# Kernel optimization log

Hardware: AMD Instinct MI355X
Metric: run time of the kernel (lower is better)

Reference implementation:

```python
import jax, jax.numpy as jnp
import numpy as np
import math

B, S, D, H = 4, 2048, 1024, 16
HD = D // H  # 64
MOD_DIMS = [("text", 768, 2048), ("image", 1024, 1024), ("audio", 512, 1500), ("video", 2048, 512)]
M = len(MOD_DIMS)
WIN, DEPTH = 3, 8


def _cantor_routes():
    coords = []
    for i in range(M):
        x = i / max(1, M - 1)
        x = max(1e-06, min(x, 1.0 - 1e-06))
        val, f = 0.0, 0.5
        for _ in range(DEPTH):
            x *= 3.0
            d = int(x)
            x -= d
            if d == 2:
                val += f
            f *= 0.5
        coords.append(val)
    c = np.asarray(coords, dtype=np.float32)
    dist = np.abs(c[:, None] - c[None, :])
    # topk smallest distances (stable tie-break like torch ascending sort)
    return np.argsort(dist, axis=1, kind="stable")[:, :WIN]

ROUTES = jnp.asarray(_cantor_routes())


def setup_inputs() -> dict:
    key = jax.random.key(0)
    ks = iter(jax.random.split(key, 32))
    inp = {}
    for name, dim, sl in MOD_DIMS:
        inp[name] = jax.random.normal(next(ks), (B, sl, dim), dtype=jnp.float32)
        inp[f"W_{name}"] = jax.random.normal(next(ks), (D, dim), dtype=jnp.float32) / math.sqrt(dim)
        inp[f"b_{name}"] = jnp.zeros((D,), dtype=jnp.float32)
    inp["mod_emb"] = jax.random.normal(next(ks), (M, D), dtype=jnp.float32) * 0.02
    for nm in ("q", "k", "v", "o"):
        inp[f"W{nm}"] = jax.random.normal(next(ks), (D, D), dtype=jnp.float32) / math.sqrt(D)
        inp[f"b{nm}"] = jnp.zeros((D,), dtype=jnp.float32)
    inp["temperature"] = jnp.asarray(0.07, dtype=jnp.float32)
    return inp


def reference(text, image, audio, video, W_text, b_text, W_image, b_image,
              W_audio, b_audio, W_video, b_video, mod_emb, Wq, bq, Wk, bk,
              Wv, bv, Wo, bo, temperature):
    xs = [text, image, audio, video]
    Ws = [W_text, W_image, W_audio, W_video]
    bs = [b_text, b_image, b_audio, b_video]
    projected = []
    for i in range(M):
        p = xs[i] @ Ws[i].T + bs[i] + mod_emb[i]          # [B, s_i, D]
        p = jnp.pad(p, ((0, 0), (0, S - p.shape[1]), (0, 0)))
        projected.append(p)
    stacked = jnp.stack(projected, axis=1)                # [B, M, S, D]

    def heads(x, W, b):
        return (x @ W.T + b).reshape(B, M, S, H, HD).transpose(0, 3, 1, 2, 4)  # [B,H,M,S,HD]

    Q = heads(stacked, Wq, bq)
    K = heads(stacked, Wk, bk)
    V = heads(stacked, Wv, bv)

    Kn = K[:, :, ROUTES]
    Vn = V[:, :, ROUTES]
    scores = jnp.einsum('bhmsd,bhmwsd->bhmsw', Q, Kn) / (math.sqrt(HD) * jnp.abs(temperature))
    attn = jax.nn.softmax(scores, axis=-1)                # dropout is identity at eval
    out = jnp.einsum('bhmsw,bhmwsd->bhmsd', attn, Vn)     # [B,H,M,S,HD]
    fused = out.mean(axis=2)                              # [B,H,S,HD]
    fused = fused.transpose(0, 2, 1, 3).reshape(B, S, D)
    return fused @ Wo.T + bo
```

## Files before the change

### kernel.cpp

```cpp
#include <hip/hip_runtime.h>

typedef unsigned short u16;
typedef __bf16 bf16x8 __attribute__((ext_vector_type(8)));
typedef u16   u16x8  __attribute__((ext_vector_type(8)));
typedef u16   u16x4  __attribute__((ext_vector_type(4)));
typedef float f32x4  __attribute__((ext_vector_type(4)));

#define RPB 5084
#define SL0 2048
#define SL1 1024
#define SL2 1500
#define SL3 512

__device__ __forceinline__ u16 f2bf(float f) {
  union { float f; unsigned u; } x; x.f = f;
  unsigned u = x.u;
  u += 0x7fffu + ((u >> 16) & 1u);
  return (u16)(u >> 16);
}
__device__ __forceinline__ float bf2f(u16 h) {
  union { unsigned u; float f; } x; x.u = ((unsigned)h) << 16;
  return x.f;
}
__device__ __forceinline__ void gll16(const u16* g, u16* l) {
  __builtin_amdgcn_global_load_lds(
      (const __attribute__((address_space(1))) void*)g,
      (__attribute__((address_space(3))) void*)l, 16, 0, 0);
}

#define NSEG 12
struct CvtSegs {
  const float* src[NSEG];
  u16*         dst[NSEG];
  int          blk_end[NSEG];
  int          blk_base[NSEG];
};
__global__ __launch_bounds__(256) void cvt_multi(CvtSegs segs) {
  int blk = blockIdx.x, seg = 0;
#pragma unroll
  for (int s = 0; s < NSEG; ++s) if (blk >= segs.blk_end[s]) seg = s + 1;
  const float* src = segs.src[seg];
  u16* dst = segs.dst[seg];
  int i = (blk - segs.blk_base[seg]) * 1024 + threadIdx.x * 4;
  f32x4 v = *(const f32x4*)(src + i);
  u16x4 o;
  o[0] = f2bf(v[0]); o[1] = f2bf(v[1]); o[2] = f2bf(v[2]); o[3] = f2bf(v[3]);
  *(u16x4*)(dst + i) = o;
}


template<int STORE_F32>
__global__ __launch_bounds__(256) void gemm_lds(
    const u16* __restrict__ A,
    const u16* __restrict__ B0, const u16* __restrict__ B1, const u16* __restrict__ B2,
    const float* __restrict__ c0, const float* __restrict__ c1, const float* __restrict__ c2,
    void* __restrict__ Cout, int Mr, int K, int ldc)
{
  __shared__ u16 lA0[128 * 32], lA1[128 * 32];
  __shared__ u16 lB0[128 * 32], lB1[128 * 32];
  const int tid  = threadIdx.x;
  const int lane = tid & 63;
  const int wave = tid >> 6;
  const int wr   = (wave >> 1) * 64;
  const int wc   = (wave & 1) * 64;
  const int row0 = blockIdx.y * 128;

  const int wsel = blockIdx.x >> 3;
  const int colL = (blockIdx.x & 7) * 128;
  const u16*   Bw   = (wsel == 0) ? B0 : (wsel == 1) ? B1 : B2;
  const float* bias = (wsel == 0) ? c0 : (wsel == 1) ? c1 : c2;

  const int sr  = wave * 32 + (lane >> 2);
  const int sc  = (lane & 3) * 8;
  int ra0 = row0 + sr;      if (ra0 >= Mr) ra0 = Mr - 1;
  int ra1 = row0 + sr + 16; if (ra1 >= Mr) ra1 = Mr - 1;
  const u16* pA0 = A + (size_t)ra0 * K + sc;
  const u16* pA1 = A + (size_t)ra1 * K + sc;
  const u16* pB0 = Bw + (size_t)(colL + sr) * K + sc;
  const u16* pB1 = pB0 + (size_t)16 * K;
  u16* dA0a = &lA0[(wave * 32) * 32];      u16* dA1a = &lA0[(wave * 32 + 16) * 32];
  u16* dA0b = &lA1[(wave * 32) * 32];      u16* dA1b = &lA1[(wave * 32 + 16) * 32];
  u16* dB0a = &lB0[(wave * 32) * 32];      u16* dB1a = &lB0[(wave * 32 + 16) * 32];
  u16* dB0b = &lB1[(wave * 32) * 32];      u16* dB1b = &lB1[(wave * 32 + 16) * 32];

  f32x4 acc[4][4];
#pragma unroll
  for (int i = 0; i < 4; ++i)
#pragma unroll
    for (int j = 0; j < 4; ++j) acc[i][j] = f32x4{0.f, 0.f, 0.f, 0.f};

  const int fr = lane & 15;
  const int fk = (lane >> 4) * 8;

  for (int k0 = 0; k0 < K; k0 += 64) {
    __syncthreads();
    gll16(pA0 + k0, dA0a);       gll16(pA1 + k0, dA1a);
    gll16(pB0 + k0, dB0a);       gll16(pB1 + k0, dB1a);
    gll16(pA0 + k0 + 32, dA0b);  gll16(pA1 + k0 + 32, dA1b);
    gll16(pB0 + k0 + 32, dB0b);  gll16(pB1 + k0 + 32, dB1b);
    __syncthreads();

    bf16x8 af[4], bfr[4];
#pragma unroll
    for (int i = 0; i < 4; ++i)
      af[i] = *(const bf16x8*)&lA0[(wr + i * 16 + fr) * 32 + fk];
#pragma unroll
    for (int j = 0; j < 4; ++j)
      bfr[j] = *(const bf16x8*)&lB0[(wc + j * 16 + fr) * 32 + fk];
#pragma unroll
    for (int i = 0; i < 4; ++i)
#pragma unroll
      for (int j = 0; j < 4; ++j)
        acc[i][j] = __builtin_amdgcn_mfma_f32_16x16x32_bf16(af[i], bfr[j], acc[i][j], 0, 0, 0);
#pragma unroll
    for (int i = 0; i < 4; ++i)
      af[i] = *(const bf16x8*)&lA1[(wr + i * 16 + fr) * 32 + fk];
#pragma unroll
    for (int j = 0; j < 4; ++j)
      bfr[j] = *(const bf16x8*)&lB1[(wc + j * 16 + fr) * 32 + fk];
#pragma unroll
    for (int i = 0; i < 4; ++i)
#pragma unroll
      for (int j = 0; j < 4; ++j)
        acc[i][j] = __builtin_amdgcn_mfma_f32_16x16x32_bf16(af[i], bfr[j], acc[i][j], 0, 0, 0);
  }

  const int fc = lane & 15;
  const int rq = (lane >> 4) * 4;
#pragma unroll
  for (int i = 0; i < 4; ++i) {
#pragma unroll
    for (int j = 0; j < 4; ++j) {
      const int cl = wc + j * 16 + fc;
      const float badd = bias[colL + cl];
      const int gc = blockIdx.x * 128 + cl;
#pragma unroll
      for (int reg = 0; reg < 4; ++reg) {
        int gr = row0 + wr + i * 16 + rq + reg;
        if (gr < Mr) {
          float v = acc[i][j][reg] + badd;
          if (STORE_F32) ((float*)Cout)[(size_t)gr * ldc + gc] = v;
          else           ((u16*)Cout)[(size_t)gr * ldc + gc] = f2bf(v);
        }
      }
    }
  }
}

struct ProjSegs {
  const u16*   A[4];
  const u16*   Bw[4];
  const float* b0[4];
  const float* b1[4];
  int Mr[4], K[4], sl[4], obase[4];
  int blk_end[4];
};
__global__ __launch_bounds__(256) void gemm_proj_all(ProjSegs ps, u16* __restrict__ Cout) {
  int blk = blockIdx.x, seg = 0;
#pragma unroll
  for (int s = 0; s < 3; ++s) if (blk >= ps.blk_end[s]) seg = s + 1;
  const int base  = seg ? ps.blk_end[seg - 1] : 0;
  const int local = blk - base;
  const int row0  = (local >> 3) * 128;
  const int col0  = (local & 7) * 128;
  const int Mr = ps.Mr[seg], K = ps.K[seg], sl = ps.sl[seg], obase = ps.obase[seg];
  const u16* A  = ps.A[seg];
  const u16* Bw = ps.Bw[seg];
  const float* bias0 = ps.b0[seg];
  const float* bias1 = ps.b1[seg];

  __shared__ u16 lA0[128 * 32], lA1[128 * 32];
  __shared__ u16 lB0[128 * 32], lB1[128 * 32];
  const int tid  = threadIdx.x;
  const int lane = tid & 63;
  const int wave = tid >> 6;
  const int wr   = (wave >> 1) * 64;
  const int wc   = (wave & 1) * 64;

  const int sr  = wave * 32 + (lane >> 2);
  const int sc  = (lane & 3) * 8;
  int ra0 = row0 + sr;      if (ra0 >= Mr) ra0 = Mr - 1;
  int ra1 = row0 + sr + 16; if (ra1 >= Mr) ra1 = Mr - 1;
  const u16* pA0 = A + (size_t)ra0 * K + sc;
  const u16* pA1 = A + (size_t)ra1 * K + sc;
  const u16* pB0 = Bw + (size_t)(col0 + sr) * K + sc;
  const u16* pB1 = pB0 + (size_t)16 * K;
  u16* dA0a = &lA0[(wave * 32) * 32];      u16* dA1a = &lA0[(wave * 32 + 16) * 32];
  u16* dA0b = &lA1[(wave * 32) * 32];      u16* dA1b = &lA1[(wave * 32 + 16) * 32];
  u16* dB0a = &lB0[(wave * 32) * 32];      u16* dB1a = &lB0[(wave * 32 + 16) * 32];
  u16* dB0b = &lB1[(wave * 32) * 32];      u16* dB1b = &lB1[(wave * 32 + 16) * 32];

  f32x4 acc[4][4];
#pragma unroll
  for (int i = 0; i < 4; ++i)
#pragma unroll
    for (int j = 0; j < 4; ++j) acc[i][j] = f32x4{0.f, 0.f, 0.f, 0.f};

  const int fr = lane & 15;
  const int fk = (lane >> 4) * 8;

  for (int k0 = 0; k0 < K; k0 += 64) {
    __syncthreads();
    gll16(pA0 + k0, dA0a);       gll16(pA1 + k0, dA1a);
    gll16(pB0 + k0, dB0a);       gll16(pB1 + k0, dB1a);
    gll16(pA0 + k0 + 32, dA0b);  gll16(pA1 + k0 + 32, dA1b);
    gll16(pB0 + k0 + 32, dB0b);  gll16(pB1 + k0 + 32, dB1b);
    __syncthreads();

    bf16x8 af[4], bfr[4];
#pragma unroll
    for (int i = 0; i < 4; ++i)
      af[i] = *(const bf16x8*)&lA0[(wr + i * 16 + fr) * 32 + fk];
#pragma unroll
    for (int j = 0; j < 4; ++j)
      bfr[j] = *(const bf16x8*)&lB0[(wc + j * 16 + fr) * 32 + fk];
#pragma unroll
    for (int i = 0; i < 4; ++i)
#pragma unroll
      for (int j = 0; j < 4; ++j)
        acc[i][j] = __builtin_amdgcn_mfma_f32_16x16x32_bf16(af[i], bfr[j], acc[i][j], 0, 0, 0);
#pragma unroll
    for (int i = 0; i < 4; ++i)
      af[i] = *(const bf16x8*)&lA1[(wr + i * 16 + fr) * 32 + fk];
#pragma unroll
    for (int j = 0; j < 4; ++j)
      bfr[j] = *(const bf16x8*)&lB1[(wc + j * 16 + fr) * 32 + fk];
#pragma unroll
    for (int i = 0; i < 4; ++i)
#pragma unroll
      for (int j = 0; j < 4; ++j)
        acc[i][j] = __builtin_amdgcn_mfma_f32_16x16x32_bf16(af[i], bfr[j], acc[i][j], 0, 0, 0);
  }

  const int fc = lane & 15;
  const int rq = (lane >> 4) * 4;
#pragma unroll
  for (int i = 0; i < 4; ++i) {
#pragma unroll
    for (int j = 0; j < 4; ++j) {
      const int c = col0 + wc + j * 16 + fc;
      const float badd = bias0[c] + bias1[c];
#pragma unroll
      for (int reg = 0; reg < 4; ++reg) {
        int gr = row0 + wr + i * 16 + rq + reg;
        if (gr < Mr) {
          int bb = gr / sl, ss = gr - bb * sl;
          Cout[(size_t)(bb * RPB + obase + ss) * 1024 + c] = f2bf(acc[i][j][reg] + badd);
        }
      }
    }
  }
}

__global__ __launch_bounds__(256) void attn_fuse(
    const u16* __restrict__ QKV,
    u16* __restrict__ fused,
    const float* __restrict__ bq, const float* __restrict__ bk, const float* __restrict__ bv,
    const float* __restrict__ temp_ptr)
{
  const int ROUTE[4][3] = {{0,1,2},{0,1,2},{2,3,0},{3,2,0}};
  const int SLm[4]  = {SL0, SL1, SL2, SL3};
  const int OFFS[4] = {0, 2048, 3072, 4572};
  const int tid  = threadIdx.x;
  const int lane = tid & 63;
  const int wave = tid >> 6;
  const int bs   = blockIdx.x * 2 + (wave >> 1);
  const int s    = bs & 2047;
  const int b    = bs >> 11;
  const int h    = (wave & 1) * 8 + (lane >> 3);
  const int sub  = lane & 7;
  const int dbase = h * 64 + sub * 8;
  const float scale = 1.0f / (8.0f * fabsf(temp_ptr[0]));

  float qf[4][8], kf[4][8], vf[4][8];
#pragma unroll
  for (int r = 0; r < 4; ++r) {
    if (s < SLm[r]) {
      const u16* base = QKV + ((size_t)(b * RPB + OFFS[r] + s)) * 3072 + dbase;
      u16x8 q8 = *(const u16x8*)(base);
      u16x8 k8 = *(const u16x8*)(base + 1024);
      u16x8 v8 = *(const u16x8*)(base + 2048);
#pragma unroll
      for (int i = 0; i < 8; ++i) {
        qf[r][i] = bf2f(q8[i]); kf[r][i] = bf2f(k8[i]); vf[r][i] = bf2f(v8[i]);
      }
    } else {
#pragma unroll
      for (int i = 0; i < 8; ++i) {
        qf[r][i] = bq[dbase + i]; kf[r][i] = bk[dbase + i]; vf[r][i] = bv[dbase + i];
      }
    }
  }

  float acc[8];
#pragma unroll
  for (int i = 0; i < 8; ++i) acc[i] = 0.f;

#pragma unroll
  for (int m = 0; m < 4; ++m) {
    float sc[3];
#pragma unroll
    for (int w = 0; w < 3; ++w) {
      const int r = ROUTE[m][w];
      float d = 0.f;
#pragma unroll
      for (int i = 0; i < 8; ++i) d += qf[m][i] * kf[r][i];
      d += __shfl_xor(d, 1, 64);
      d += __shfl_xor(d, 2, 64);
      d += __shfl_xor(d, 4, 64);
      sc[w] = d * scale;
    }
    float mx = fmaxf(sc[0], fmaxf(sc[1], sc[2]));
    float e0 = __expf(sc[0] - mx), e1 = __expf(sc[1] - mx), e2 = __expf(sc[2] - mx);
    float inv = 1.0f / (e0 + e1 + e2);
    float ws[3] = {e0 * inv, e1 * inv, e2 * inv};
#pragma unroll
    for (int w = 0; w < 3; ++w) {
      const int r = ROUTE[m][w];
#pragma unroll
      for (int i = 0; i < 8; ++i) acc[i] += ws[w] * vf[r][i];
    }
  }
  u16x8 o;
#pragma unroll
  for (int i = 0; i < 8; ++i) o[i] = f2bf(acc[i] * 0.25f);
  *(u16x8*)(fused + (size_t)bs * 1024 + dbase) = o;
}

extern "C" void kernel_launch(void* const* d_in, const int* in_sizes, int n_in,
                              void* d_out, int out_size, void* d_ws, size_t ws_size,
                              hipStream_t stream) {
  const int B = 4, S = 2048, D = 1024;
  const int SL[4]   = {SL0, SL1, SL2, SL3};
  const int DIM[4]  = {768, 1024, 512, 2048};
  const int OFFS[4] = {0, 2048, 3072, 4572};

  const float* x[4]  = {(const float*)d_in[0], (const float*)d_in[3], (const float*)d_in[6], (const float*)d_in[9]};
  const float* Wm[4] = {(const float*)d_in[1], (const float*)d_in[4], (const float*)d_in[7], (const float*)d_in[10]};
  const float* bm[4] = {(const float*)d_in[2], (const float*)d_in[5], (const float*)d_in[8], (const float*)d_in[11]};
  const float* mod_emb = (const float*)d_in[12];
  const float* Wq = (const float*)d_in[13]; const float* bq = (const float*)d_in[14];
  const float* Wk = (const float*)d_in[15]; const float* bk = (const float*)d_in[16];
  const float* Wv = (const float*)d_in[17]; const float* bv = (const float*)d_in[18];
  const float* Wo = (const float*)d_in[19]; const float* bo = (const float*)d_in[20];
  const float* temp = (const float*)d_in[21];

  const int RROWS = B * RPB;
  const size_t stackedB = ((size_t)RROWS * D * 2 + 255) / 256 * 256;
  const size_t qkvB     = ((size_t)RROWS * 3 * D * 2 + 255) / 256 * 256;
  const size_t wB       = ((size_t)D * D * 2 + 255) / 256 * 256;
  size_t wmB[4];
  for (int m = 0; m < 4; ++m) wmB[m] = ((size_t)D * DIM[m] * 2 + 255) / 256 * 256;
  const size_t need = stackedB + qkvB + 4 * wB + wmB[0] + wmB[1] + wmB[2] + wmB[3];
  if (ws_size < need) return;

  char* p = (char*)d_ws;
  u16* stacked = (u16*)p;  p += stackedB;
  char* qkvbase = p;
  u16* qkv     = (u16*)p;  p += qkvB;
  u16* wqb     = (u16*)p;  p += wB;
  u16* wkb     = (u16*)p;  p += wB;
  u16* wvb     = (u16*)p;  p += wB;
  u16* wob     = (u16*)p;  p += wB;
  u16* wmb[4];
  for (int m = 0; m < 4; ++m) { wmb[m] = (u16*)p; p += wmB[m]; }
  u16* fusedb  = stacked;

  u16* xb[4];
  {
    char* q = qkvbase;
    for (int m = 0; m < 4; ++m) {
      xb[m] = (u16*)q;
      q += ((size_t)B * SL[m] * DIM[m] * 2 + 255) / 256 * 256;
    }
  }

  {
    CvtSegs cs;
    const float* srcs[NSEG] = {x[0], x[1], x[2], x[3], Wm[0], Wm[1], Wm[2], Wm[3], Wq, Wk, Wv, Wo};
    u16* dsts[NSEG] = {xb[0], xb[1], xb[2], xb[3], wmb[0], wmb[1], wmb[2], wmb[3], wqb, wkb, wvb, wob};
    int ns[NSEG];
    for (int m = 0; m < 4; ++m) ns[m] = B * SL[m] * DIM[m];
    for (int m = 0; m < 4; ++m) ns[4 + m] = D * DIM[m];
    for (int i = 0; i < 4; ++i) ns[8 + i] = D * D;
    int base = 0;
    for (int i = 0; i < NSEG; ++i) {
      cs.src[i] = srcs[i]; cs.dst[i] = dsts[i];
      cs.blk_base[i] = base;
      base += (ns[i] + 1023) / 1024;
      cs.blk_end[i] = base;
    }
    cvt_multi<<<base, 256, 0, stream>>>(cs);
  }

  {
    const int ord[4] = {3, 1, 0, 2};
    ProjSegs ps;
    int base = 0;
    for (int i = 0; i < 4; ++i) {
      int m = ord[i];
      int Mr = B * SL[m];
      ps.A[i] = xb[m]; ps.Bw[i] = wmb[m];
      ps.b0[i] = bm[m]; ps.b1[i] = mod_emb + m * D;
      ps.Mr[i] = Mr; ps.K[i] = DIM[m]; ps.sl[i] = SL[m]; ps.obase[i] = OFFS[m];
      base += 8 * ((Mr + 127) / 128);
      ps.blk_end[i] = base;
    }
    gemm_proj_all<<<base, 256, 0, stream>>>(ps, stacked);
  }

  {
    dim3 grid(24, (RROWS + 127) / 128);
    gemm_lds<0><<<grid, 256, 0, stream>>>(stacked, wqb, wkb, wvb, bq, bk, bv,
                                          qkv, RROWS, D, 3 * D);
  }

  attn_fuse<<<(B * S) / 2, 256, 0, stream>>>(qkv, fusedb, bq, bk, bv, temp);

  {
    dim3 grid(8, (B * S) / 128);
    gemm_lds<1><<<grid, 256, 0, stream>>>(fusedb, wob, wob, wob, bo, bo, bo,
                                          d_out, B * S, D, D);
  }
}
```

Measured before the change: 474.2 us.

## Add 256x256-tile QKV GEMM kernel with 4-slot LDS pipeline

```diff
diff --git a/kernel.cpp b/kernel.cpp
--- a/kernel.cpp
+++ b/kernel.cpp
@@ -47,7 +47,6 @@
   o[0] = f2bf(v[0]); o[1] = f2bf(v[1]); o[2] = f2bf(v[2]); o[3] = f2bf(v[3]);
   *(u16x4*)(dst + i) = o;
 }
-
 
 template<int STORE_F32>
 __global__ __launch_bounds__(256) void gemm_lds(
@@ -142,6 +141,107 @@
           if (STORE_F32) ((float*)Cout)[(size_t)gr * ldc + gc] = v;
           else           ((u16*)Cout)[(size_t)gr * ldc + gc] = f2bf(v);
         }
+      }
+    }
+  }
+}
+
+__global__ __launch_bounds__(512, 2) void gemm_qkv_256(
+    const u16* __restrict__ A,
+    const u16* __restrict__ B0, const u16* __restrict__ B1, const u16* __restrict__ B2,
+    const float* __restrict__ c0, const float* __restrict__ c1, const float* __restrict__ c2,
+    u16* __restrict__ C, int Mr, int K)
+{
+  __shared__ u16 lds[4][2][8192];
+  const int tid  = threadIdx.x;
+  const int lane = tid & 63;
+  const int wave = tid >> 6;
+  const int wm   = wave >> 2;
+  const int wn   = wave & 3;
+  const int row0 = blockIdx.y * 256;
+  const int cb   = blockIdx.x;
+  const int wsel = cb >> 2;
+  const int colL = (cb & 3) * 256;
+  const u16*   Bw   = (wsel == 0) ? B0 : (wsel == 1) ? B1 : B2;
+  const float* bias = (wsel == 0) ? c0 : (wsel == 1) ? c1 : c2;
+
+  const int srow = lane >> 2;
+  const int soct = (lane & 3) * 8;
+  int ra0 = row0 + wave * 16 + srow;        if (ra0 >= Mr) ra0 = Mr - 1;
+  int ra1 = row0 + 128 + wave * 16 + srow;  if (ra1 >= Mr) ra1 = Mr - 1;
+  const u16* pA0 = A + (size_t)ra0 * K + soct;
+  const u16* pA1 = A + (size_t)ra1 * K + soct;
+  const u16* pB0 = Bw + (size_t)(colL + wave * 16 + srow) * K + soct;
+  const u16* pB1 = pB0 + (size_t)128 * K;
+  const int NS = K >> 5;
+
+#define QSTAGE(slot, k0) do {                                   \
+    gll16(pA0 + (k0), (u16*)&lds[slot][0][wave * 512]);         \
+    gll16(pA1 + (k0), (u16*)&lds[slot][0][4096 + wave * 512]);  \
+    gll16(pB0 + (k0), (u16*)&lds[slot][1][wave * 512]);         \
+    gll16(pB1 + (k0), (u16*)&lds[slot][1][4096 + wave * 512]);  \
+  } while (0)
+
+  f32x4 acc[8][4];
+#pragma unroll
+  for (int m = 0; m < 8; ++m)
+#pragma unroll
+    for (int n = 0; n < 4; ++n) acc[m][n] = f32x4{0.f, 0.f, 0.f, 0.f};
+
+  QSTAGE(0, 0);
+  QSTAGE(1, 32);
+  QSTAGE(2, 64);
+
+  const int fr = lane & 15;
+  const int hk = (lane >> 4) * 8;
+
+#pragma unroll 4
+  for (int s = 0; s < NS; ++s) {
+    asm volatile("s_waitcnt vmcnt(8)" ::: "memory");
+    __builtin_amdgcn_s_barrier();
+
+    const u16* Ab = &lds[s & 3][0][0];
+    const u16* Bb = &lds[s & 3][1][0];
+    bf16x8 af[8], bf[4];
+#pragma unroll
+    for (int m = 0; m < 8; ++m)
+      af[m] = *(const bf16x8*)&Ab[(wm * 128 + m * 16 + fr) * 32 + hk];
+#pragma unroll
+    for (int n = 0; n < 4; ++n)
+      bf[n] = *(const bf16x8*)&Bb[(wn * 64 + n * 16 + fr) * 32 + hk];
+
+    const int s3 = s + 3;
+    const int k3 = (s3 < NS ? s3 : NS - 1) << 5;
+    QSTAGE(s3 & 3, k3);
+
+    asm volatile("s_waitcnt lgkmcnt(0)" ::: "memory");
+    __builtin_amdgcn_sched_barrier(0);
+    __builtin_amdgcn_s_setprio(1);
+#pragma unroll
+    for (int m = 0; m < 8; ++m)
+#pragma unroll
+      for (int n = 0; n < 4; ++n)
+        acc[m][n] = __builtin_amdgcn_mfma_f32_16x16x32_bf16(af[m], bf[n], acc[m][n], 0, 0, 0);
+    __builtin_amdgcn_s_setprio(0);
+  }
+#undef QSTAGE
+
+  asm volatile("s_waitcnt vmcnt(0)" ::: "memory");
+
+  const int fc = lane & 15;
+  const int rq = (lane >> 4) * 4;
+#pragma unroll
+  for (int m = 0; m < 8; ++m) {
+#pragma unroll
+    for (int n = 0; n < 4; ++n) {
+      const int cl = wn * 64 + n * 16 + fc;
+      const float badd = bias[colL + cl];
+      const int gc = cb * 256 + cl;
+#pragma unroll
+      for (int reg = 0; reg < 4; ++reg) {
+        int gr = row0 + wm * 128 + m * 16 + rq + reg;
+        if (gr < Mr)
+          C[(size_t)gr * 3072 + gc] = f2bf(acc[m][n][reg] + badd);
       }
     }
   }
@@ -410,9 +510,9 @@
   }
 
   {
-    dim3 grid(24, (RROWS + 127) / 128);
-    gemm_lds<0><<<grid, 256, 0, stream>>>(stacked, wqb, wkb, wvb, bq, bk, bv,
-                                          qkv, RROWS, D, 3 * D);
+    dim3 grid(12, (RROWS + 255) / 256);
+    gemm_qkv_256<<<grid, 512, 0, stream>>>(stacked, wqb, wkb, wvb, bq, bk, bv,
+                                           qkv, RROWS, D);
   }
 
   attn_fuse<<<(B * S) / 2, 256, 0, stream>>>(qkv, fusedb, bq, bk, bv, temp);
```

Result: no change. 478.2 us (+0.8%).
